# Kernel tuning notes

Measured on AMD Instinct MI355X. Metric: run time of the kernel, lower is better.

Reference implementation:

```python
import jax, jax.numpy as jnp
import numpy as np
import math

B, S, E = 2, 2048, 1024
A, H, F, L = 1024, 16, 4096, 4
DH = A // H  # per-head dim = 64
EPS = 1e-5


def _positional_encoding(max_len, d_model):
    pe = np.zeros((max_len, d_model), dtype=np.float32)
    pos = np.arange(max_len, dtype=np.float32)[:, None]
    div = np.exp(np.arange(0, d_model, 2, dtype=np.float32) * -(math.log(10000.0) / d_model))
    pe[:, 0::2] = np.sin(pos * div)
    pe[:, 1::2] = np.cos(pos * div)
    return jnp.asarray(pe)


def setup_inputs() -> dict:
    key = jax.random.key(0)
    ks = jax.random.split(key, 16)
    std = 0.02
    x = jax.random.normal(ks[0], (B, S, E), dtype=jnp.float32)
    pe = _positional_encoding(S, E)
    Wq = jax.random.normal(ks[1], (L, H, E, DH), dtype=jnp.float32) * std
    bq = jnp.zeros((L, H, DH), dtype=jnp.float32)
    Wk = jax.random.normal(ks[2], (L, H, E, DH), dtype=jnp.float32) * std
    bk = jnp.zeros((L, H, DH), dtype=jnp.float32)
    Wv = jax.random.normal(ks[3], (L, H, E, DH), dtype=jnp.float32) * std
    bv = jnp.zeros((L, H, DH), dtype=jnp.float32)
    Wo = jax.random.normal(ks[4], (L, A, E), dtype=jnp.float32) * std
    bo = jnp.zeros((L, E), dtype=jnp.float32)
    ln1_g = jnp.ones((L, E), dtype=jnp.float32)
    ln1_b = jnp.zeros((L, E), dtype=jnp.float32)
    ln2_g = jnp.ones((L, E), dtype=jnp.float32)
    ln2_b = jnp.zeros((L, E), dtype=jnp.float32)
    ff_W1 = jax.random.normal(ks[5], (L, E, F), dtype=jnp.float32) * std
    ff_b1 = jnp.zeros((L, F), dtype=jnp.float32)
    ff_W2 = jax.random.normal(ks[6], (L, F, E), dtype=jnp.float32) * std
    ff_b2 = jnp.zeros((L, E), dtype=jnp.float32)
    return dict(x=x, pe=pe, Wq=Wq, bq=bq, Wk=Wk, bk=bk, Wv=Wv, bv=bv,
                Wo=Wo, bo=bo, ln1_g=ln1_g, ln1_b=ln1_b, ln2_g=ln2_g, ln2_b=ln2_b,
                ff_W1=ff_W1, ff_b1=ff_b1, ff_W2=ff_W2, ff_b2=ff_b2)


def _layernorm(x, g, b):
    mu = jnp.mean(x, axis=-1, keepdims=True)
    var = jnp.mean(jnp.square(x - mu), axis=-1, keepdims=True)
    return (x - mu) * jax.lax.rsqrt(var + EPS) * g + b


def reference(x, pe, Wq, bq, Wk, bk, Wv, bv, Wo, bo,
              ln1_g, ln1_b, ln2_g, ln2_b, ff_W1, ff_b1, ff_W2, ff_b2):
    x = x + pe[None, :x.shape[1]]
    scale = 1.0 / math.sqrt(DH)  # torch divides by dk**0.5, dk = per-head attention_dim
    for l in range(L):
        # batched per-head projections (equivalent to the per-head Linear loop)
        q = jnp.einsum('bse,hed->bhsd', x, Wq[l]) + bq[l][None, :, None, :]
        k = jnp.einsum('bse,hed->bhsd', x, Wk[l]) + bk[l][None, :, None, :]
        v = jnp.einsum('bse,hed->bhsd', x, Wv[l]) + bv[l][None, :, None, :]
        scores = jnp.einsum('bhsd,bhtd->bhst', q, k) * scale
        p = jax.nn.softmax(scores, axis=-1)
        o = jnp.einsum('bhst,bhtd->bhsd', p, v)  # [B,H,S,DH]
        o = o.transpose(0, 2, 1, 3).reshape(x.shape[0], x.shape[1], A)  # concat heads
        attn = o @ Wo[l] + bo[l]
        x = _layernorm(x + attn, ln1_g[l], ln1_b[l])
        h = jax.nn.relu(x @ ff_W1[l] + ff_b1[l])
        ff = h @ ff_W2[l] + ff_b2[l]
        x = _layernorm(x + ff, ln2_g[l], ln2_b[l])
    return x
```

## Files before the change

### kernel.cpp

```cpp
#include <hip/hip_runtime.h>

#define DEV __device__ __forceinline__

typedef __attribute__((ext_vector_type(8))) short s8v;
typedef __attribute__((ext_vector_type(4))) short s4v;
typedef __attribute__((ext_vector_type(4))) float f4v;
typedef __attribute__((ext_vector_type(2))) unsigned int u2v;

#define BB 2
#define SS 2048
#define EE 1024
#define AA 1024
#define HH 16
#define FF 4096
#define LL 4
#define DHD 64
#define MM (BB*SS)

DEV float b2f(short s){
  union { unsigned int u; float f; } v; v.u = ((unsigned int)(unsigned short)s) << 16; return v.f;
}
DEV short f2b(float f){
  unsigned int u = __float_as_uint(f);
  unsigned int r = (u + 0x7FFFu + ((u >> 16) & 1u)) >> 16;
  return (short)(unsigned short)r;
}
DEV unsigned int cvtpk(float lo, float hi){
  unsigned int r; asm("v_cvt_pk_bf16_f32 %0, %1, %2" : "=v"(r) : "v"(lo), "v"(hi)); return r;
}
DEV float vexp2(float x){ float r; asm("v_exp_f32 %0, %1" : "=v"(r) : "v"(x)); return r; }
DEV void gld16(const void* g, void* l){
  __builtin_amdgcn_global_load_lds((const __attribute__((address_space(1))) unsigned int*)g,
                                   (__attribute__((address_space(3))) unsigned int*)l,
                                   16, 0, 0);
}
DEV f4v fzero(){ f4v v; v[0]=0.f; v[1]=0.f; v[2]=0.f; v[3]=0.f; return v; }
DEV int swz64(int row, int col){ return row*64 + (col ^ ((row&7)<<3)); }

__global__ __launch_bounds__(256) void add_pe_k(const float* __restrict__ x, const float* __restrict__ pe,
                                                short* __restrict__ xb){
  size_t g = ((size_t)blockIdx.x*256 + threadIdx.x) * 4;
  f4v xv = *(const f4v*)(x + g);
  f4v pv = *(const f4v*)(pe + (g & (size_t)(SS*EE - 1)));
  s4v ob;
  #pragma unroll
  for (int j=0;j<4;j++) ob[j] = f2b(xv[j] + pv[j]);
  *(s4v*)(xb + g) = ob;
}

__global__ __launch_bounds__(256) void transpose_f2b(const float* __restrict__ in, short* __restrict__ out,
                                                     int R, int C){
  __shared__ short t[32][36];
  int tx = threadIdx.x, ty = threadIdx.y;
  int rt = blockIdx.y*32, ct = blockIdx.x*32;
  size_t zb = (size_t)blockIdx.z * R * C;
  f4v v = *(const f4v*)(in + zb + (size_t)(rt+ty)*C + ct + tx*4);
  #pragma unroll
  for (int j=0;j<4;j++) t[tx*4+j][ty] = f2b(v[j]);
  __syncthreads();
  s4v ov;
  #pragma unroll
  for (int j=0;j<4;j++) ov[j] = t[ty][tx*4+j];
  *(s4v*)(out + zb + (size_t)(ct+ty)*R + rt + tx*4) = ov;
}

__global__ __launch_bounds__(256) void transpose_qkv(const float* __restrict__ Wq, const float* __restrict__ Wk,
                                                     const float* __restrict__ Wv, short* __restrict__ out){
  __shared__ short t[32][36];
  int tx = threadIdx.x, ty = threadIdx.y;
  int rt = blockIdx.y*32, ct = blockIdx.x*32;
  int z = blockIdx.z;
  const float* in = (z < 16 ? Wq : (z < 32 ? Wk : Wv));
  size_t zb = (size_t)(z & 15) * EE * DHD;
  f4v v = *(const f4v*)(in + zb + (size_t)(rt+ty)*DHD + ct + tx*4);
  #pragma unroll
  for (int j=0;j<4;j++) t[tx*4+j][ty] = f2b(v[j]);
  __syncthreads();
  s4v ov;
  #pragma unroll
  for (int j=0;j<4;j++) ov[j] = t[ty][tx*4+j];
  *(s4v*)(out + (size_t)z*DHD*EE + (size_t)(ct+ty)*EE + rt + tx*4) = ov;
}

__global__ __launch_bounds__(256) void vt_k(const short* __restrict__ qkv, short* __restrict__ Vt){
  __shared__ short t[32][36];
  int tx = threadIdx.x, ty = threadIdx.y;
  int t0 = blockIdx.x*32, d0 = blockIdx.y*32, bh = blockIdx.z;
  int b = bh >> 4, h = bh & 15;
  const short* src = qkv + (size_t)b*SS*3*AA + 2*AA + h*64;
  s4v v = *(const s4v*)(src + (size_t)(t0+ty)*3*AA + d0 + tx*4);
  #pragma unroll
  for (int j=0;j<4;j++) t[tx*4+j][ty] = v[j];
  __syncthreads();
  s4v ov;
  #pragma unroll
  for (int j=0;j<4;j++) ov[j] = t[ty][tx*4+j];
  *(s4v*)(Vt + ((size_t)bh*64 + d0 + ty)*SS + t0 + tx*4) = ov;
}

__global__ void concat_bias(const float* __restrict__ bq, const float* __restrict__ bk,
                            const float* __restrict__ bv, float* __restrict__ out){
  int i = blockIdx.x*256 + threadIdx.x;
  float v = (i < AA) ? bq[i] : (i < 2*AA ? bk[i-AA] : bv[i-2*AA]);
  out[i] = v;
}

template<int BM, int BN, int OUTMODE>
__global__ __launch_bounds__(256) void gemm_bt(const short* __restrict__ Ag, const short* __restrict__ Btg,
                                               const float* __restrict__ bias, short* __restrict__ Cout,
                                               int M, int N, int K){
  constexpr int WM = BM/2, WN = BN/2;
  constexpr int MI = WM/16, NI = WN/16;
  constexpr int ACH = BM/16, BCH = BN/16, TCH = ACH + BCH, CPW = TCH/4;
  __shared__ __attribute__((aligned(16))) short As[2][BM*32];
  __shared__ __attribute__((aligned(16))) short Bs[2][BN*32];
  const int tid = threadIdx.x;
  const int wave = tid >> 6, lane = tid & 63;
  const int wr = wave >> 1, wc = wave & 1;
  const int l15 = lane & 15, l4 = lane >> 4;

  const int gx = gridDim.x;
  const int nwg = gx * gridDim.y;
  const int w0 = blockIdx.y * gx + blockIdx.x;
  const int q8 = nwg >> 3, r8 = nwg & 7;
  const int xcd = w0 & 7, pos = w0 >> 3;
  const int lg = (xcd < r8 ? xcd*(q8+1) : r8*(q8+1) + (xcd-r8)*q8) + pos;
  const int bn = (lg % gx) * BN, bm = (lg / gx) * BM;

  const int lrow = lane >> 2;
  const int lcol = ((lane & 3) ^ ((lane >> 3) & 3)) * 8;
  const int fslot = (l4 ^ ((l15 >> 1) & 3)) * 8;

  f4v acc[MI][NI];
  #pragma unroll
  for (int i=0;i<MI;i++)
    #pragma unroll
    for (int j=0;j<NI;j++) acc[i][j] = fzero();

#define STAGE_TILE(pb, kt) \
  { _Pragma("unroll") \
    for (int c = 0; c < CPW; c++){ \
      int ch = wave * CPW + c; \
      if (ch < ACH){ \
        gld16(Ag + (size_t)(bm + ch*16 + lrow)*K + (kt) + lcol, &As[pb][ch*512]); \
      } else { \
        gld16(Btg + (size_t)(bn + (ch-ACH)*16 + lrow)*K + (kt) + lcol, &Bs[pb][(ch-ACH)*512]); \
      } \
    } }

#define COMPUTE_TILE(pb) \
  { s8v af[MI], bfr[NI]; \
    _Pragma("unroll") \
    for (int mi=0;mi<MI;mi++) af[mi] = *(const s8v*)&As[pb][(wr*WM + mi*16 + l15)*32 + fslot]; \
    _Pragma("unroll") \
    for (int ni=0;ni<NI;ni++) bfr[ni] = *(const s8v*)&Bs[pb][(wc*WN + ni*16 + l15)*32 + fslot]; \
    _Pragma("unroll") \
    for (int mi=0;mi<MI;mi++) \
      _Pragma("unroll") \
      for (int ni=0;ni<NI;ni++) \
        acc[mi][ni] = __builtin_amdgcn_mfma_f32_16x16x32_bf16(af[mi], bfr[ni], acc[mi][ni], 0,0,0); }

  STAGE_TILE(0, 0);
  __syncthreads();
  int cur = 0;
  for (int kt = 32; kt < K; kt += 32){
    STAGE_TILE(cur^1, kt);
    COMPUTE_TILE(cur);
    __syncthreads();
    cur ^= 1;
  }
  COMPUTE_TILE(cur);

#undef STAGE_TILE
#undef COMPUTE_TILE

  #pragma unroll
  for (int mi=0;mi<MI;mi++){
    int row = bm + wr*WM + mi*16 + l4*4;
    #pragma unroll
    for (int ni=0;ni<NI;ni++){
      int col = bn + wc*WN + ni*16 + l15;
      float bv = bias[col];
      #pragma unroll
      for (int r=0;r<4;r++){
        float v = acc[mi][ni][r] + bv;
        if constexpr (OUTMODE==1) v = fmaxf(v, 0.f);
        Cout[(size_t)(row+r)*N + col] = f2b(v);
      }
    }
  }
}

__global__ __launch_bounds__(256) void gemm_sk(const short* __restrict__ Ag0, const short* __restrict__ Btg0,
                                               const float* __restrict__ bias, short* __restrict__ Cout0,
                                               int M, int N, int Kfull){
  constexpr int BM = 64, BN = 128;
  constexpr int WM = BM/2, WN = BN/2;
  constexpr int MI = WM/16, NI = WN/16;
  constexpr int ACH = BM/16, BCH = BN/16, TCH = ACH + BCH, CPW = TCH/4;
  __shared__ __attribute__((aligned(16))) short As[2][BM*32];
  __shared__ __attribute__((aligned(16))) short Bs[2][BN*32];
  const int tid = threadIdx.x;
  const int wave = tid >> 6, lane = tid & 63;
  const int wr = wave >> 1, wc = wave & 1;
  const int l15 = lane & 15, l4 = lane >> 4;

  const int kz = blockIdx.z;
  const int Kh = Kfull >> 1;
  const short* Ag  = Ag0  + (size_t)kz * Kh;
  const short* Btg = Btg0 + (size_t)kz * Kh;
  short* Cout = Cout0 + (size_t)kz * M * N;

  const int gx = gridDim.x;
  const int nwg = gx * gridDim.y;
  const int w0 = blockIdx.y * gx + blockIdx.x;
  const int q8 = nwg >> 3, r8 = nwg & 7;
  const int xcd = w0 & 7, pos = w0 >> 3;
  const int lg = (xcd < r8 ? xcd*(q8+1) : r8*(q8+1) + (xcd-r8)*q8) + pos;
  const int bn = (lg % gx) * BN, bm = (lg / gx) * BM;

  const int lrow = lane >> 2;
  const int lcol = ((lane & 3) ^ ((lane >> 3) & 3)) * 8;
  const int fslot = (l4 ^ ((l15 >> 1) & 3)) * 8;

  f4v acc[MI][NI];
  #pragma unroll
  for (int i=0;i<MI;i++)
    #pragma unroll
    for (int j=0;j<NI;j++) acc[i][j] = fzero();

#define STAGE_TILE(pb, kt) \
  { _Pragma("unroll") \
    for (int c = 0; c < CPW; c++){ \
      int ch = wave * CPW + c; \
      if (ch < ACH){ \
        gld16(Ag + (size_t)(bm + ch*16 + lrow)*Kfull + (kt) + lcol, &As[pb][ch*512]); \
      } else { \
        gld16(Btg + (size_t)(bn + (ch-ACH)*16 + lrow)*Kfull + (kt) + lcol, &Bs[pb][(ch-ACH)*512]); \
      } \
    } }

#define COMPUTE_TILE(pb) \
  { s8v af[MI], bfr[NI]; \
    _Pragma("unroll") \
    for (int mi=0;mi<MI;mi++) af[mi] = *(const s8v*)&As[pb][(wr*WM + mi*16 + l15)*32 + fslot]; \
    _Pragma("unroll") \
    for (int ni=0;ni<NI;ni++) bfr[ni] = *(const s8v*)&Bs[pb][(wc*WN + ni*16 + l15)*32 + fslot]; \
    _Pragma("unroll") \
    for (int mi=0;mi<MI;mi++) \
      _Pragma("unroll") \
      for (int ni=0;ni<NI;ni++) \
        acc[mi][ni] = __builtin_amdgcn_mfma_f32_16x16x32_bf16(af[mi], bfr[ni], acc[mi][ni], 0,0,0); }

  STAGE_TILE(0, 0);
  __syncthreads();
  int cur = 0;
  for (int kt = 32; kt < Kh; kt += 32){
    STAGE_TILE(cur^1, kt);
    COMPUTE_TILE(cur);
    __syncthreads();
    cur ^= 1;
  }
  COMPUTE_TILE(cur);

#undef STAGE_TILE
#undef COMPUTE_TILE

  #pragma unroll
  for (int mi=0;mi<MI;mi++){
    int row = bm + wr*WM + mi*16 + l4*4;
    #pragma unroll
    for (int ni=0;ni<NI;ni++){
      int col = bn + wc*WN + ni*16 + l15;
      float bv = (kz == 0) ? bias[col] : 0.f;
      #pragma unroll
      for (int r=0;r<4;r++){
        float v = acc[mi][ni][r] + bv;
        Cout[(size_t)(row+r)*N + col] = f2b(v);
      }
    }
  }
}

template<int OUTMODE>
__global__ __launch_bounds__(512) void gemm256(const short* __restrict__ Ag, const short* __restrict__ Btg,
                                               const float* __restrict__ bias, short* __restrict__ Cout,
                                               int M, int N, int K){
  __shared__ __attribute__((aligned(16))) short As[4][256*32];
  __shared__ __attribute__((aligned(16))) short Bs[4][256*32];
  const int tid = threadIdx.x;
  const int wave = tid >> 6, lane = tid & 63;
  const int wm = wave >> 2, wn = wave & 3;
  const int l15 = lane & 15, l4 = lane >> 4;

  const int gx = gridDim.x;
  const int nwg = gx * gridDim.y;
  const int w0 = blockIdx.y * gx + blockIdx.x;
  const int q8 = nwg >> 3, r8 = nwg & 7;
  const int xcd = w0 & 7, pos = w0 >> 3;
  const int lg = (xcd < r8 ? xcd*(q8+1) : r8*(q8+1) + (xcd-r8)*q8) + pos;
  const int bn = (lg % gx) * 256, bm = (lg / gx) * 256;

  const int srow = wave*16 + (lane >> 2);
  const int scol = ((lane & 3) ^ ((lane >> 3) & 3)) * 8;
  const int fslot = (l4 ^ ((l15 >> 1) & 3)) * 8;

  f4v acc[8][4];
  #pragma unroll
  for (int i=0;i<8;i++)
    #pragma unroll
    for (int j=0;j<4;j++) acc[i][j] = fzero();

#define STG_A(bb, kt, r) gld16(Ag + (size_t)(bm + (r)*128 + srow)*K + (kt) + scol, &As[bb][((r)*128 + wave*16)*32]);
#define STG_B(bb, kt, r) gld16(Btg + (size_t)(bn + (r)*128 + srow)*K + (kt) + scol, &Bs[bb][((r)*128 + wave*16)*32]);
#define AFRAG(bb, j) (*(const s8v*)&As[bb][((wm*128) + (j)*16 + l15)*32 + fslot])
#define BFRAG(bb, n) (*(const s8v*)&Bs[bb][((wn*64) + (n)*16 + l15)*32 + fslot])
#define MPHASE(bb, j0, a0, a1) \
    { __builtin_amdgcn_s_setprio(1); \
      _Pragma("unroll") \
      for (int n=0;n<4;n++){ \
        acc[j0][n]   = __builtin_amdgcn_mfma_f32_16x16x32_bf16(a0, bf[n], acc[j0][n], 0,0,0); \
        acc[j0+1][n] = __builtin_amdgcn_mfma_f32_16x16x32_bf16(a1, bf[n], acc[j0+1][n], 0,0,0); \
      } \
      __builtin_amdgcn_s_setprio(0); }

  const int NT = K >> 5;
  STG_A(0,0,0); STG_A(0,0,1); STG_B(0,0,0); STG_B(0,0,1);
  STG_A(1,32,0); STG_A(1,32,1); STG_B(1,32,0); STG_B(1,32,1);
  STG_A(2,64,0); STG_A(2,64,1); STG_B(2,64,0); STG_B(2,64,1);

  for (int t = 0; t < NT; ++t){
    const int b = t & 3;
    const int sb = (t+3) & 3;
    const bool st = (t+3) < NT;
    const int kt3 = (t+3)*32;
    if (t+2 < NT)      asm volatile("s_waitcnt vmcnt(8)\n\ts_barrier" ::: "memory");
    else if (t+1 < NT) asm volatile("s_waitcnt vmcnt(4)\n\ts_barrier" ::: "memory");
    else               asm volatile("s_waitcnt vmcnt(0)\n\ts_barrier" ::: "memory");

    s8v bf[4];
    #pragma unroll
    for (int n=0;n<4;n++) bf[n] = BFRAG(b, n);

    if (st){ STG_A(sb, kt3, 0); }
    { s8v a0 = AFRAG(b,0), a1 = AFRAG(b,1); MPHASE(b, 0, a0, a1); }
    if (st){ STG_A(sb, kt3, 1); }
    { s8v a0 = AFRAG(b,2), a1 = AFRAG(b,3); MPHASE(b, 2, a0, a1); }
    if (st){ STG_B(sb, kt3, 0); }
    { s8v a0 = AFRAG(b,4), a1 = AFRAG(b,5); MPHASE(b, 4, a0, a1); }
    if (st){ STG_B(sb, kt3, 1); }
    { s8v a0 = AFRAG(b,6), a1 = AFRAG(b,7); MPHASE(b, 6, a0, a1); }
  }
#undef STG_A
#undef STG_B
#undef AFRAG
#undef BFRAG
#undef MPHASE

  #pragma unroll
  for (int mi=0;mi<8;mi++){
    int row = bm + wm*128 + mi*16 + l4*4;
    #pragma unroll
    for (int ni=0;ni<4;ni++){
      int col = bn + wn*64 + ni*16 + l15;
      float bv = bias[col];
      #pragma unroll
      for (int r=0;r<4;r++){
        float v = acc[mi][ni][r] + bv;
        if constexpr (OUTMODE==1) v = fmaxf(v, 0.f);
        Cout[(size_t)(row+r)*N + col] = f2b(v);
      }
    }
  }
}

__global__ __launch_bounds__(512) void attn_k(const short* __restrict__ qkv, const short* __restrict__ Vt,
                                              short* __restrict__ o){
  __shared__ __attribute__((aligned(16))) short Kls[64*64];
  __shared__ __attribute__((aligned(16))) short Vls[2][64*64];
  __shared__ __attribute__((aligned(16))) short Pls[8][16][68];
  const int tid = threadIdx.x, wave = tid>>6, lane = tid&63;
  const int l15 = lane&15, l4 = lane>>4;
  const int w0 = blockIdx.y*16 + blockIdx.x;
  const int idx = w0 >> 3;
  const int bh = (w0 & 7)*4 + (idx >> 4);
  const int qb = idx & 15;
  const int b = bh >> 4, h = bh & 15;
  const size_t rs = 3*AA;
  const short* qbase = qkv + (size_t)b*SS*rs + h*64;
  const short* kbase = qbase + AA;
  const short* vtb   = Vt + (size_t)bh*64*SS;
  const int m0 = qb*128 + wave*16;

  const float QSC = 0.125f * 1.44269504f;
  s8v aq0 = *(const s8v*)(qbase + (size_t)(m0 + l15)*rs + l4*8);
  s8v aq1 = *(const s8v*)(qbase + (size_t)(m0 + l15)*rs + 32 + l4*8);
  #pragma unroll
  for (int j=0;j<8;j++){ aq0[j] = f2b(b2f(aq0[j])*QSC); aq1[j] = f2b(b2f(aq1[j])*QSC); }

  f4v oacc[4];
  #pragma unroll
  for (int df=0;df<4;df++) oacc[df] = fzero();
  float lrow = 0.f;

  const int srow = tid >> 3, scol = (tid & 7) * 8;
  s8v kst, vst;

#define LOADKV(t0) \
  kst = *(const s8v*)(kbase + (size_t)((t0)+srow)*rs + scol); \
  vst = *(const s8v*)(vtb + (size_t)srow*SS + (t0) + scol);
#define WRITEK() \
  *(s8v*)&Kls[swz64(srow, scol)] = kst;
#define WRITEV(pb) \
  *(s8v*)&Vls[pb][swz64(srow, scol)] = vst;

  LOADKV(0); WRITEK(); WRITEV(0);
  __syncthreads();

  for (int t0=0; t0<SS; t0+=64){
    const int cur = (t0>>6)&1;
    const bool more = (t0+64 < SS);
    if (more){ LOADKV(t0+64); }

    f4v sacc[4];
    #pragma unroll
    for (int f=0; f<4; f++){
      s8v k0 = *(const s8v*)&Kls[swz64(f*16+l15, l4*8)];
      s8v k1 = *(const s8v*)&Kls[swz64(f*16+l15, 32+l4*8)];
      f4v s = fzero();
      s = __builtin_amdgcn_mfma_f32_16x16x32_bf16(k0, aq0, s, 0,0,0);
      sacc[f] = __builtin_amdgcn_mfma_f32_16x16x32_bf16(k1, aq1, s, 0,0,0);
    }
    __syncthreads();
    if (more){ WRITEK(); WRITEV(cur^1); }

    float rsum = 0.f;
    #pragma unroll
    for (int f=0; f<4; f++){
      #pragma unroll
      for (int r=0; r<4; r++){
        float p = vexp2(sacc[f][r]);
        sacc[f][r] = p; rsum += p;
      }
    }
    rsum += __shfl_xor(rsum, 16);
    rsum += __shfl_xor(rsum, 32);
    lrow += rsum;

    #pragma unroll
    for (int f=0; f<4; f++){
      u2v q;
      q[0] = cvtpk(sacc[f][0], sacc[f][1]);
      q[1] = cvtpk(sacc[f][2], sacc[f][3]);
      *(u2v*)&Pls[wave][l15][f*16 + l4*4] = q;
    }

    s8v ap0 = *(const s8v*)&Pls[wave][l15][l4*8];
    s8v ap1 = *(const s8v*)&Pls[wave][l15][32 + l4*8];
    #pragma unroll
    for (int df=0; df<4; df++){
      s8v v0 = *(const s8v*)&Vls[cur][swz64(df*16+l15, l4*8)];
      s8v v1 = *(const s8v*)&Vls[cur][swz64(df*16+l15, 32+l4*8)];
      oacc[df] = __builtin_amdgcn_mfma_f32_16x16x32_bf16(v0, ap0, oacc[df], 0,0,0);
      oacc[df] = __builtin_amdgcn_mfma_f32_16x16x32_bf16(v1, ap1, oacc[df], 0,0,0);
    }
    __syncthreads();
  }
#undef LOADKV
#undef WRITEK
#undef WRITEV

  float rl = 1.f / lrow;
  short* orow = o + (size_t)(b*SS + m0 + l15)*AA + h*64;
  #pragma unroll
  for (int df=0; df<4; df++){
    u2v q;
    q[0] = cvtpk(oacc[df][0]*rl, oacc[df][1]*rl);
    q[1] = cvtpk(oacc[df][2]*rl, oacc[df][3]*rl);
    *(u2v*)&orow[df*16 + l4*4] = q;
  }
}

template<int MODE>
__global__ __launch_bounds__(256) void ln_fused(const short* __restrict__ y1, const short* __restrict__ y2,
                                                const float* __restrict__ gg, const float* __restrict__ bb,
                                                short* __restrict__ xb, float* __restrict__ fo){
  const int row = blockIdx.x, tid = threadIdx.x;
  size_t base = (size_t)row*EE + tid*4;
  s4v a = *(const s4v*)(y1 + base);
  s4v c = *(const s4v*)(y2 + base);
  f4v y;
  #pragma unroll
  for (int j=0;j<4;j++) y[j] = b2f(a[j]) + b2f(c[j]);
  float s  = y[0]+y[1]+y[2]+y[3];
  float sq = y[0]*y[0]+y[1]*y[1]+y[2]*y[2]+y[3]*y[3];
  #pragma unroll
  for (int msk=1; msk<64; msk<<=1){ s += __shfl_xor(s, msk); sq += __shfl_xor(sq, msk); }
  __shared__ float red[8];
  int wave = tid>>6;
  if ((tid&63)==0){ red[wave]=s; red[4+wave]=sq; }
  __syncthreads();
  s  = red[0]+red[1]+red[2]+red[3];
  sq = red[4]+red[5]+red[6]+red[7];
  float mu  = s * (1.f/EE);
  float var = sq * (1.f/EE) - mu*mu;
  float rstd = rsqrtf(var + 1e-5f);
  f4v ov; s4v ob;
  #pragma unroll
  for (int j=0;j<4;j++){
    int ccol = tid*4 + j;
    float v = (y[j]-mu)*rstd*gg[ccol] + bb[ccol];
    ov[j]=v; ob[j]=f2b(v);
  }
  *(s4v*)(xb + base) = ob;
  if constexpr (MODE==1) *(f4v*)(fo + base) = ov;
}

template<int MODE>
__global__ __launch_bounds__(256) void ln_fused2(const short* __restrict__ y1a, const short* __restrict__ y1b,
                                                 const short* __restrict__ y2,
                                                 const float* __restrict__ gg, const float* __restrict__ bb,
                                                 short* __restrict__ xb, float* __restrict__ fo){
  const int row = blockIdx.x, tid = threadIdx.x;
  size_t base = (size_t)row*EE + tid*4;
  s4v a  = *(const s4v*)(y1a + base);
  s4v a2 = *(const s4v*)(y1b + base);
  s4v c  = *(const s4v*)(y2 + base);
  f4v y;
  #pragma unroll
  for (int j=0;j<4;j++) y[j] = b2f(a[j]) + b2f(a2[j]) + b2f(c[j]);
  float s  = y[0]+y[1]+y[2]+y[3];
  float sq = y[0]*y[0]+y[1]*y[1]+y[2]*y[2]+y[3]*y[3];
  #pragma unroll
  for (int msk=1; msk<64; msk<<=1){ s += __shfl_xor(s, msk); sq += __shfl_xor(sq, msk); }
  __shared__ float red[8];
  int wave = tid>>6;
  if ((tid&63)==0){ red[wave]=s; red[4+wave]=sq; }
  __syncthreads();
  s  = red[0]+red[1]+red[2]+red[3];
  sq = red[4]+red[5]+red[6]+red[7];
  float mu  = s * (1.f/EE);
  float var = sq * (1.f/EE) - mu*mu;
  float rstd = rsqrtf(var + 1e-5f);
  f4v ov; s4v ob;
  #pragma unroll
  for (int j=0;j<4;j++){
    int ccol = tid*4 + j;
    float v = (y[j]-mu)*rstd*gg[ccol] + bb[ccol];
    ov[j]=v; ob[j]=f2b(v);
  }
  *(s4v*)(xb + base) = ob;
  if constexpr (MODE==1) *(f4v*)(fo + base) = ov;
}

extern "C" void kernel_launch(void* const* d_in, const int* in_sizes, int n_in,
                              void* d_out, int out_size, void* d_ws, size_t ws_size,
                              hipStream_t stream){
  const float* x   = (const float*)d_in[0];
  const float* pe  = (const float*)d_in[1];
  const float* Wq  = (const float*)d_in[2];
  const float* bq  = (const float*)d_in[3];
  const float* Wk  = (const float*)d_in[4];
  const float* bk  = (const float*)d_in[5];
  const float* Wv  = (const float*)d_in[6];
  const float* bv  = (const float*)d_in[7];
  const float* Wo  = (const float*)d_in[8];
  const float* bo  = (const float*)d_in[9];
  const float* g1  = (const float*)d_in[10];
  const float* be1 = (const float*)d_in[11];
  const float* g2  = (const float*)d_in[12];
  const float* be2 = (const float*)d_in[13];
  const float* W1  = (const float*)d_in[14];
  const float* fb1 = (const float*)d_in[15];
  const float* W2  = (const float*)d_in[16];
  const float* fb2 = (const float*)d_in[17];

  char* wsp = (char*)d_ws;
  short* xb   = (short*)wsp;  wsp += (size_t)MM*EE*2;
  short* act  = (short*)wsp;  wsp += (size_t)MM*FF*2;
  short* ob   = (short*)wsp;  wsp += (size_t)MM*AA*2;
  short* tmpb = (short*)wsp;  wsp += (size_t)2*MM*EE*2;
  short* wT   = (short*)wsp;  wsp += (size_t)FF*EE*2;
  float* bqkv = (float*)wsp;  wsp += 3*AA*4;
  short* qkv  = act;
  short* Vtb  = act + (size_t)MM*3*AA;
  short* hid  = act;
  short* tmpb2 = tmpb + (size_t)MM*EE;

  add_pe_k<<<(MM*EE)/(256*4), 256, 0, stream>>>(x, pe, xb);

  dim3 tb2(8,32);
  for (int l=0; l<LL; l++){
    transpose_qkv<<<dim3(DHD/32, EE/32, 48), tb2, 0, stream>>>(Wq + (size_t)l*HH*EE*DHD,
                                                               Wk + (size_t)l*HH*EE*DHD,
                                                               Wv + (size_t)l*HH*EE*DHD, wT);
    concat_bias<<<12, 256, 0, stream>>>(bq + l*AA, bk + l*AA, bv + l*AA, bqkv);
    gemm_bt<128,128,0><<<dim3(3*AA/128, MM/128), 256, 0, stream>>>(xb, wT, bqkv, qkv, MM, 3*AA, EE);
    vt_k<<<dim3(SS/32, DHD/32, BB*HH), tb2, 0, stream>>>(qkv, Vtb);
    attn_k<<<dim3(SS/128, BB*HH), 512, 0, stream>>>(qkv, Vtb, ob);
    transpose_f2b<<<dim3(EE/32, AA/32, 1), tb2, 0, stream>>>(Wo + (size_t)l*AA*EE, wT, AA, EE);
    gemm_bt<64,128,0><<<dim3(EE/128, MM/64), 256, 0, stream>>>(ob, wT, bo + l*EE, tmpb, MM, EE, AA);
    ln_fused<0><<<MM, 256, 0, stream>>>(tmpb, xb, g1 + l*EE, be1 + l*EE, xb, nullptr);
    transpose_f2b<<<dim3(FF/32, EE/32, 1), tb2, 0, stream>>>(W1 + (size_t)l*EE*FF, wT, EE, FF);
    gemm256<1><<<dim3(FF/256, MM/256), 512, 0, stream>>>(xb, wT, fb1 + l*FF, hid, MM, FF, EE);
    transpose_f2b<<<dim3(EE/32, FF/32, 1), tb2, 0, stream>>>(W2 + (size_t)l*FF*EE, wT, FF, EE);
    gemm_sk<<<dim3(EE/128, MM/64, 2), 256, 0, stream>>>(hid, wT, fb2 + l*EE, tmpb, MM, EE, FF);
    if (l == LL-1)
      ln_fused2<1><<<MM, 256, 0, stream>>>(tmpb, tmpb2, xb, g2 + l*EE, be2 + l*EE, xb, (float*)d_out);
    else
      ln_fused2<0><<<MM, 256, 0, stream>>>(tmpb, tmpb2, xb, g2 + l*EE, be2 + l*EE, xb, nullptr);
  }
}
```

Before: 984.6 us.

## Triple-buffer split-K GEMM with interleaved loads and single barrier per tile

Rewrites the split-K GEMM main loop to use three LDS buffers, prefetching two tiles ahead. Global-to-LDS loads for the next stage are interleaved between MFMA groups, and each iteration uses one manual vmcnt wait plus barrier instead of two syncthreads. MFMA sections are wrapped in s_setprio raises. This aims to hide memory latency better, at the cost of more LDS per block and a hand-tuned waitcnt count that must match the number of loads issued per stage.

After: 1.008 ms. +2.4%, slower.

```diff
diff --git a/kernel.cpp b/kernel.cpp
--- a/kernel.cpp
+++ b/kernel.cpp
@@ -194,12 +194,8 @@
 __global__ __launch_bounds__(256) void gemm_sk(const short* __restrict__ Ag0, const short* __restrict__ Btg0,
                                                const float* __restrict__ bias, short* __restrict__ Cout0,
                                                int M, int N, int Kfull){
-  constexpr int BM = 64, BN = 128;
-  constexpr int WM = BM/2, WN = BN/2;
-  constexpr int MI = WM/16, NI = WN/16;
-  constexpr int ACH = BM/16, BCH = BN/16, TCH = ACH + BCH, CPW = TCH/4;
-  __shared__ __attribute__((aligned(16))) short As[2][BM*32];
-  __shared__ __attribute__((aligned(16))) short Bs[2][BN*32];
+  __shared__ __attribute__((aligned(16))) short As[3][64*32];
+  __shared__ __attribute__((aligned(16))) short Bs[3][128*32];
   const int tid = threadIdx.x;
   const int wave = tid >> 6, lane = tid & 63;
   const int wr = wave >> 1, wc = wave & 1;
@@ -217,61 +213,63 @@
   const int q8 = nwg >> 3, r8 = nwg & 7;
   const int xcd = w0 & 7, pos = w0 >> 3;
   const int lg = (xcd < r8 ? xcd*(q8+1) : r8*(q8+1) + (xcd-r8)*q8) + pos;
-  const int bn = (lg % gx) * BN, bm = (lg / gx) * BM;
+  const int bn = (lg % gx) * 128, bm = (lg / gx) * 64;
 
   const int lrow = lane >> 2;
   const int lcol = ((lane & 3) ^ ((lane >> 3) & 3)) * 8;
   const int fslot = (l4 ^ ((l15 >> 1) & 3)) * 8;
 
-  f4v acc[MI][NI];
-  #pragma unroll
-  for (int i=0;i<MI;i++)
-    #pragma unroll
-    for (int j=0;j<NI;j++) acc[i][j] = fzero();
-
-#define STAGE_TILE(pb, kt) \
-  { _Pragma("unroll") \
-    for (int c = 0; c < CPW; c++){ \
-      int ch = wave * CPW + c; \
-      if (ch < ACH){ \
-        gld16(Ag + (size_t)(bm + ch*16 + lrow)*Kfull + (kt) + lcol, &As[pb][ch*512]); \
-      } else { \
-        gld16(Btg + (size_t)(bn + (ch-ACH)*16 + lrow)*Kfull + (kt) + lcol, &Bs[pb][(ch-ACH)*512]); \
-      } \
-    } }
-
-#define COMPUTE_TILE(pb) \
-  { s8v af[MI], bfr[NI]; \
-    _Pragma("unroll") \
-    for (int mi=0;mi<MI;mi++) af[mi] = *(const s8v*)&As[pb][(wr*WM + mi*16 + l15)*32 + fslot]; \
-    _Pragma("unroll") \
-    for (int ni=0;ni<NI;ni++) bfr[ni] = *(const s8v*)&Bs[pb][(wc*WN + ni*16 + l15)*32 + fslot]; \
-    _Pragma("unroll") \
-    for (int mi=0;mi<MI;mi++) \
-      _Pragma("unroll") \
-      for (int ni=0;ni<NI;ni++) \
-        acc[mi][ni] = __builtin_amdgcn_mfma_f32_16x16x32_bf16(af[mi], bfr[ni], acc[mi][ni], 0,0,0); }
-
-  STAGE_TILE(0, 0);
-  __syncthreads();
-  int cur = 0;
-  for (int kt = 32; kt < Kh; kt += 32){
-    STAGE_TILE(cur^1, kt);
-    COMPUTE_TILE(cur);
-    __syncthreads();
-    cur ^= 1;
-  }
-  COMPUTE_TILE(cur);
-
-#undef STAGE_TILE
-#undef COMPUTE_TILE
-
-  #pragma unroll
-  for (int mi=0;mi<MI;mi++){
-    int row = bm + wr*WM + mi*16 + l4*4;
-    #pragma unroll
-    for (int ni=0;ni<NI;ni++){
-      int col = bn + wc*WN + ni*16 + l15;
+  f4v acc[2][4];
+  #pragma unroll
+  for (int i=0;i<2;i++)
+    #pragma unroll
+    for (int j=0;j<4;j++) acc[i][j] = fzero();
+
+#define STG(bb, kt, c) \
+  { int ch = (c)*4 + wave; \
+    if (ch < 4) gld16(Ag + (size_t)(bm + ch*16 + lrow)*Kfull + (kt) + lcol, &As[bb][ch*512]); \
+    else        gld16(Btg + (size_t)(bn + (ch-4)*16 + lrow)*Kfull + (kt) + lcol, &Bs[bb][(ch-4)*512]); }
+#define AFRG(bb, mi) (*(const s8v*)&As[bb][(wr*32 + (mi)*16 + l15)*32 + fslot])
+
+  const int NT = Kh >> 5;
+  STG(0,0,0); STG(0,0,1); STG(0,0,2);
+  STG(1,32,0); STG(1,32,1); STG(1,32,2);
+
+  for (int t = 0; t < NT; ++t){
+    const int b = t % 3;
+    const int sb = (t+2) % 3;
+    const bool st = (t+2) < NT;
+    const int kt2 = (t+2)*32;
+    if (t+1 < NT) asm volatile("s_waitcnt vmcnt(3)\n\ts_barrier" ::: "memory");
+    else          asm volatile("s_waitcnt vmcnt(0)\n\ts_barrier" ::: "memory");
+
+    s8v bf[4];
+    #pragma unroll
+    for (int n=0;n<4;n++) bf[n] = *(const s8v*)&Bs[b][(wc*64 + n*16 + l15)*32 + fslot];
+
+    if (st){ STG(sb, kt2, 0); }
+    { s8v af = AFRG(b,0);
+      __builtin_amdgcn_s_setprio(1);
+      #pragma unroll
+      for (int n=0;n<4;n++) acc[0][n] = __builtin_amdgcn_mfma_f32_16x16x32_bf16(af, bf[n], acc[0][n], 0,0,0);
+      __builtin_amdgcn_s_setprio(0); }
+    if (st){ STG(sb, kt2, 1); }
+    { s8v af = AFRG(b,1);
+      __builtin_amdgcn_s_setprio(1);
+      #pragma unroll
+      for (int n=0;n<4;n++) acc[1][n] = __builtin_amdgcn_mfma_f32_16x16x32_bf16(af, bf[n], acc[1][n], 0,0,0);
+      __builtin_amdgcn_s_setprio(0); }
+    if (st){ STG(sb, kt2, 2); }
+  }
+#undef STG
+#undef AFRG
+
+  #pragma unroll
+  for (int mi=0;mi<2;mi++){
+    int row = bm + wr*32 + mi*16 + l4*4;
+    #pragma unroll
+    for (int ni=0;ni<4;ni++){
+      int col = bn + wc*64 + ni*16 + l15;
       float bv = (kz == 0) ? bias[col] : 0.f;
       #pragma unroll
       for (int r=0;r<4;r++){
```
